# Performance work log

Measured on AMD Instinct MI355X. Metric: run time of the kernel, lower is better.

The kernel has to match this reference:

```python
import jax, jax.numpy as jnp
import numpy as np

N_BITS = 16
BATCH = 4194304  # 2**22 tokens
TABLE_SIZE = 2 ** (N_BITS - 1)  # largest CUMULATIVE/FLIP context is n_bits-1 bits


def setup_inputs() -> dict:
    key = jax.random.key(0)
    k1, k2 = jax.random.split(key)
    # input bit tensor [batch, n_bits], values in {0,1}; index n_bits-1 is bit 0 (LSB)
    bits = jax.random.randint(k1, (BATCH, N_BITS), 0, 2, dtype=jnp.int32)
    # per-bit-position RAM lookup tables, padded to the max address space.
    # Binary contents {0,1}, stored as float32 so the flip/XOR math is expressible.
    tables = (jax.random.uniform(k2, (N_BITS, TABLE_SIZE)) < 0.5).astype(jnp.float32)
    return {"bits": bits, "tables": tables}


def reference(bits, tables):
    """BitLevelMapper forward, CUMULATIVE context + FLIP output mode.

    bits:   [B, n_bits] int32 in {0,1}, array index n_bits-1-k holds bit value k (LSB=k=0)
    tables: [n_bits, 2^(n_bits-1)] float32 in {0,1}; row i is the RAM/LUT for bit_pos i.
    For bit_pos i the context is the lowest i bits (bit0..bit_{i-1});
    address = sum_k context_bit_k * 2^k; flip = table[i, address];
    output bit i = input bit i XOR flip.
    """
    n_bits = bits.shape[1]
    bits_rev = bits[:, ::-1]                      # [B, n] column k = bit value k
    k = jnp.arange(n_bits)
    # W[i, k] = 2^k if k < i else 0  -> addr_i = sum_{k<i} bit_k * 2^k (addr_0 = 0)
    W = jnp.where(k[None, :] < k[:, None], (1 << k)[None, :], 0).astype(jnp.int32)
    addr = bits_rev @ W.T                          # [B, n] int32 RAM addresses per bit_pos
    flip = tables[k[None, :], addr]                # [B, n] gather: tables[i, addr[b, i]]
    x = bits_rev.astype(tables.dtype)
    out_rev = x + flip - 2.0 * x * flip            # XOR expressed arithmetically
    return out_rev[:, ::-1]                        # back to original bit-array layout
```

## Files before the change

kernel.cpp:

```cpp
#include <hip/hip_runtime.h>
#include <hip/hip_bf16.h>


#define PACK_WORDS 2048

__global__ __launch_bounds__(256) void
pack_tables_kernel(const float* __restrict__ tables, unsigned* __restrict__ packed) {
    int g = blockIdx.x * blockDim.x + threadIdx.x;
    bool val = false;
    if (g < 65535) {
        int i = 31 - __clz(g + 1);
        int a = g - ((1 << i) - 1);
        val = tables[i * 32768 + a] != 0.0f;
    }
    unsigned long long m = __ballot(val);
    if ((threadIdx.x & 63) == 0) {
        packed[(g >> 5)]     = (unsigned)m;
        packed[(g >> 5) + 1] = (unsigned)(m >> 32);
    }
}

__global__ __launch_bounds__(256) void
blm_kernel(const int4* __restrict__ bits4, const unsigned* __restrict__ packed,
           float4* __restrict__ out4, int nrows) {
    __shared__ unsigned tab[PACK_WORDS];
    for (int k = threadIdx.x; k < PACK_WORDS; k += 256)
        tab[k] = packed[k];
    __syncthreads();

    const int lane    = threadIdx.x & 63;
    const int wave    = (blockIdx.x * 256 + threadIdx.x) >> 6;
    const int nwaves  = (gridDim.x * 256) >> 6;
    const int nchunks = nrows >> 6;

    for (int c = wave; c < nchunks; c += nwaves) {
        const size_t base = (size_t)c * 256;

        int4 m0 = bits4[base +   0 + lane];
        int4 m1 = bits4[base +  64 + lane];
        int4 m2 = bits4[base + 128 + lane];
        int4 m3 = bits4[base + 192 + lane];

        unsigned n0 = (unsigned)((m0.x << 3) | (m0.y << 2) | (m0.z << 1) | m0.w);
        unsigned n1 = (unsigned)((m1.x << 3) | (m1.y << 2) | (m1.z << 1) | m1.w);
        unsigned n2 = (unsigned)((m2.x << 3) | (m2.y << 2) | (m2.z << 1) | m2.w);
        unsigned n3 = (unsigned)((m3.x << 3) | (m3.y << 2) | (m3.z << 1) | m3.w);
        unsigned pk = n0 | (n1 << 4) | (n2 << 8) | (n3 << 12);

        const int hi   = lane >> 4;
        const int bsrc = (lane & 15) << 2;
        unsigned v = 0;
        #pragma unroll
        for (int q = 0; q < 4; ++q) {
            unsigned x  = (unsigned)__shfl((int)pk, bsrc + q, 64);
            unsigned nb = (x >> (hi * 4)) & 0xFu;
            v |= nb << (12 - 4 * q);
        }

        unsigned r16 = 0;
        #pragma unroll
        for (int i = 0; i < 16; ++i) {
            unsigned mask = (1u << i) - 1u;
            unsigned bidx = mask + (v & mask);
            unsigned fl   = (tab[bidx >> 5] >> (bidx & 31u));
            r16 |= (((v >> i) ^ fl) & 1u) << i;
        }

        #pragma unroll
        for (int j = 0; j < 4; ++j) {
            unsigned y = (unsigned)__shfl((int)r16, (j << 4) + (lane >> 2), 64);
            int q4 = (lane & 3) << 2;
            float4 f;
            f.x = (float)((y >> (15 - q4)) & 1u);
            f.y = (float)((y >> (14 - q4)) & 1u);
            f.z = (float)((y >> (13 - q4)) & 1u);
            f.w = (float)((y >> (12 - q4)) & 1u);
            out4[base + j * 64 + lane] = f;
        }
    }
}

extern "C" void kernel_launch(void* const* d_in, const int* in_sizes, int n_in,
                              void* d_out, int out_size, void* d_ws, size_t ws_size,
                              hipStream_t stream) {
    const int*   bits   = (const int*)d_in[0];
    const float* tables = (const float*)d_in[1];
    float*       out    = (float*)d_out;
    unsigned*    packed = (unsigned*)d_ws;

    int nrows = in_sizes[0] / 16;

    pack_tables_kernel<<<65536 / 256, 256, 0, stream>>>(tables, packed);

    blm_kernel<<<8192, 256, 0, stream>>>((const int4*)bits, packed,
                                         (float4*)out, nrows);
}
```

Measured before the change: 434.9 us.

## Split mapper into compress pass and expand pass with nontemporal stores

Replaces the single fused grid-stride kernel with two kernels. The first packs each 16-bit row into a 16-bit word in workspace. The second reads those words, does the table lookups per quarter-row thread and writes float4 outputs with nontemporal stores. The goal is simpler access patterns, fewer shuffles and better store streaming. The cost is an extra kernel launch and an extra round trip of 8 MB of intermediate data through memory.

```diff
diff --git a/kernel.cpp b/kernel.cpp
--- a/kernel.cpp
+++ b/kernel.cpp
@@ -3,6 +3,8 @@
 
 
 #define PACK_WORDS 2048
+
+typedef float vfloat4 __attribute__((ext_vector_type(4)));
 
 __global__ __launch_bounds__(256) void
 pack_tables_kernel(const float* __restrict__ tables, unsigned* __restrict__ packed) {
@@ -21,77 +23,66 @@
 }
 
 __global__ __launch_bounds__(256) void
-blm_kernel(const int4* __restrict__ bits4, const unsigned* __restrict__ packed,
-           float4* __restrict__ out4, int nrows) {
+compress_kernel(const int4* __restrict__ bits4, unsigned short* __restrict__ rowv) {
+    int t = blockIdx.x * 256 + threadIdx.x;
+    int4 m = bits4[t];
+    unsigned nb = (unsigned)((m.x << 3) | (m.y << 2) | (m.z << 1) | m.w);
+    unsigned part = nb << (12 - ((t & 3) << 2));
+    part |= (unsigned)__shfl_xor((int)part, 1, 64);
+    part |= (unsigned)__shfl_xor((int)part, 2, 64);
+    if ((t & 3) == 0)
+        rowv[t >> 2] = (unsigned short)part;
+}
+
+__global__ __launch_bounds__(256) void
+expand_kernel(const unsigned short* __restrict__ rowv,
+              const unsigned* __restrict__ packed,
+              vfloat4* __restrict__ out4) {
     __shared__ unsigned tab[PACK_WORDS];
-    for (int k = threadIdx.x; k < PACK_WORDS; k += 256)
-        tab[k] = packed[k];
+    {
+        const int4* p4 = (const int4*)packed;
+        int4* t4 = (int4*)tab;
+        t4[threadIdx.x]       = p4[threadIdx.x];
+        t4[threadIdx.x + 256] = p4[threadIdx.x + 256];
+    }
     __syncthreads();
 
-    const int lane    = threadIdx.x & 63;
-    const int wave    = (blockIdx.x * 256 + threadIdx.x) >> 6;
-    const int nwaves  = (gridDim.x * 256) >> 6;
-    const int nchunks = nrows >> 6;
-
-    for (int c = wave; c < nchunks; c += nwaves) {
-        const size_t base = (size_t)c * 256;
-
-        int4 m0 = bits4[base +   0 + lane];
-        int4 m1 = bits4[base +  64 + lane];
-        int4 m2 = bits4[base + 128 + lane];
-        int4 m3 = bits4[base + 192 + lane];
-
-        unsigned n0 = (unsigned)((m0.x << 3) | (m0.y << 2) | (m0.z << 1) | m0.w);
-        unsigned n1 = (unsigned)((m1.x << 3) | (m1.y << 2) | (m1.z << 1) | m1.w);
-        unsigned n2 = (unsigned)((m2.x << 3) | (m2.y << 2) | (m2.z << 1) | m2.w);
-        unsigned n3 = (unsigned)((m3.x << 3) | (m3.y << 2) | (m3.z << 1) | m3.w);
-        unsigned pk = n0 | (n1 << 4) | (n2 << 8) | (n3 << 12);
-
-        const int hi   = lane >> 4;
-        const int bsrc = (lane & 15) << 2;
-        unsigned v = 0;
+    const size_t base = (size_t)blockIdx.x * 1024 + threadIdx.x;
+    const int q4 = (int)(threadIdx.x & 3) << 2;
+    #pragma unroll
+    for (int it = 0; it < 4; ++it) {
+        size_t t = base + (size_t)it * 256;
+        unsigned v = rowv[t >> 2];
+        float o[4];
         #pragma unroll
-        for (int q = 0; q < 4; ++q) {
-            unsigned x  = (unsigned)__shfl((int)pk, bsrc + q, 64);
-            unsigned nb = (x >> (hi * 4)) & 0xFu;
-            v |= nb << (12 - 4 * q);
-        }
-
-        unsigned r16 = 0;
-        #pragma unroll
-        for (int i = 0; i < 16; ++i) {
+        for (int j = 0; j < 4; ++j) {
+            int i = 15 - q4 - j;
             unsigned mask = (1u << i) - 1u;
             unsigned bidx = mask + (v & mask);
-            unsigned fl   = (tab[bidx >> 5] >> (bidx & 31u));
-            r16 |= (((v >> i) ^ fl) & 1u) << i;
+            unsigned fl   = tab[bidx >> 5] >> (bidx & 31u);
+            o[j] = (float)(((v >> i) ^ fl) & 1u);
         }
-
-        #pragma unroll
-        for (int j = 0; j < 4; ++j) {
-            unsigned y = (unsigned)__shfl((int)r16, (j << 4) + (lane >> 2), 64);
-            int q4 = (lane & 3) << 2;
-            float4 f;
-            f.x = (float)((y >> (15 - q4)) & 1u);
-            f.y = (float)((y >> (14 - q4)) & 1u);
-            f.z = (float)((y >> (13 - q4)) & 1u);
-            f.w = (float)((y >> (12 - q4)) & 1u);
-            out4[base + j * 64 + lane] = f;
-        }
+        vfloat4 f = {o[0], o[1], o[2], o[3]};
+        __builtin_nontemporal_store(f, &out4[t]);
     }
 }
 
 extern "C" void kernel_launch(void* const* d_in, const int* in_sizes, int n_in,
                               void* d_out, int out_size, void* d_ws, size_t ws_size,
                               hipStream_t stream) {
-    const int*   bits   = (const int*)d_in[0];
-    const float* tables = (const float*)d_in[1];
-    float*       out    = (float*)d_out;
-    unsigned*    packed = (unsigned*)d_ws;
+    const int*      bits   = (const int*)d_in[0];
+    const float*    tables = (const float*)d_in[1];
+    float*          out    = (float*)d_out;
+    unsigned*       packed = (unsigned*)d_ws;
+    unsigned short* rowv   = (unsigned short*)((char*)d_ws + 8192);
 
-    int nrows = in_sizes[0] / 16;
+    int nrows    = in_sizes[0] / 16;
+    int nquarter = nrows * 4;
 
     pack_tables_kernel<<<65536 / 256, 256, 0, stream>>>(tables, packed);
 
-    blm_kernel<<<8192, 256, 0, stream>>>((const int4*)bits, packed,
-                                         (float4*)out, nrows);
+    compress_kernel<<<nquarter / 256, 256, 0, stream>>>((const int4*)bits, rowv);
+
+    expand_kernel<<<nquarter / 1024, 256, 0, stream>>>(rowv, packed,
+                                                       (vfloat4*)out);
 }
```

Result: no change. 428.9 us (-1.4%).
